# Kernel optimization log

Hardware: AMD Instinct MI355X
Metric: run time of the kernel (lower is better)

## Reference

```python
import jax, jax.numpy as jnp
from jax import lax
import numpy as np

DN = ('NCHW', 'OIHW', 'NCHW')


def conv(x, w, b, pad=0):
    y = lax.conv_general_dilated(x, w, (1, 1), [(pad, pad), (pad, pad)],
                                 dimension_numbers=DN)
    return y + b[None, :, None, None]


def deconv(x, w, b, stride=1):
    # PyTorch ConvTranspose2d weight is (in, out, kH, kW); equivalent conv uses
    # flipped, in/out-transposed kernel with lhs dilation = stride, pad = k-1.
    k = w.shape[2]
    wt = jnp.flip(w, (2, 3)).transpose(1, 0, 2, 3)
    y = lax.conv_general_dilated(x, wt, (1, 1), [(k - 1, k - 1), (k - 1, k - 1)],
                                 lhs_dilation=(stride, stride), dimension_numbers=DN)
    return y + b[None, :, None, None]


def maxpool2(x):
    return lax.reduce_window(x, -jnp.inf, lax.max, (1, 1, 2, 2), (1, 1, 2, 2), 'VALID')


def setup_inputs() -> dict:
    key = jax.random.key(0)
    ks = jax.random.split(key, 12)
    B = 256

    def he(k, shape, fan_in):
        return jax.random.normal(k, shape, jnp.float32) * np.sqrt(2.0 / fan_in)

    inp = {
        'x': jax.random.normal(ks[0], (B, 1, 28, 28), jnp.float32),
        # encoder convs
        'w1': he(ks[1], (128, 1, 5, 5), 1 * 25), 'b1': jnp.zeros((128,), jnp.float32),
        'w2': he(ks[2], (128, 128, 5, 5), 128 * 25), 'b2': jnp.zeros((128,), jnp.float32),
        'w3': he(ks[3], (128, 128, 5, 5), 128 * 25), 'b3': jnp.zeros((128,), jnp.float32),
        # decoder transposed convs (torch shape: in, out, kH, kW)
        't1w': he(ks[4], (128, 128, 4, 4), 128 * 16), 't1b': jnp.zeros((128,), jnp.float32),
        't2w': he(ks[5], (128, 128, 4, 4), 128 * 16), 't2b': jnp.zeros((128,), jnp.float32),
        't3w': he(ks[6], (128, 128, 5, 5), 128 * 25), 't3b': jnp.zeros((128,), jnp.float32),
        't4w': he(ks[7], (128, 128, 5, 5), 128 * 25), 't4b': jnp.zeros((128,), jnp.float32),
        # mu_net 1x1 conv
        'mw': he(ks[8], (1, 128, 1, 1), 128), 'mb': jnp.zeros((1,), jnp.float32),
        # codebook: Embedding(128, 128), init ~ N(0, 1)
        'dict_w': jax.random.normal(ks[9], (128, 128), jnp.float32),
    }
    return inp


def reference(x, w1, b1, w2, b2, w3, b3,
              t1w, t1b, t2w, t2b, t3w, t3b, t4w, t4b,
              mw, mb, dict_w):
    BETA, RATE = 0.25, 5.0
    # ---- encoder ----
    h = jax.nn.relu(conv(x, w1, b1, pad=0))          # (B,128,24,24)
    h = jax.nn.relu(conv(h, w2, b2, pad=2))          # (B,128,24,24)
    h = maxpool2(h)                                  # (B,128,12,12)
    h = conv(h, w3, b3, pad=2)                       # (B,128,12,12)
    z = maxpool2(h)                                  # (B,128,6,6)

    # ---- nearest_neighbor (faithful: argmax of distance, as in the source) ----
    z_sg = lax.stop_gradient(z)
    z2 = jnp.sum(z_sg * z_sg, axis=1, keepdims=True)          # (B,1,6,6)
    w2n = jnp.sum(dict_w * dict_w, axis=1)                     # (K,)
    cross = jnp.einsum('bchw,kc->bkhw', z_sg, lax.stop_gradient(dict_w))
    d2 = z2 + w2n[None, :, None, None] - 2.0 * cross           # (B,K,6,6)
    index = jnp.argmax(d2, axis=1)                             # (B,6,6) int

    # ---- embedding gather ----
    val = dict_w[index].transpose(0, 3, 1, 2)                  # (B,128,6,6)

    # ---- decoder on detached codes ----
    f = lax.stop_gradient(val)
    f = jax.nn.relu(deconv(f, t1w, t1b, stride=1))             # (B,128,9,9)
    f = jax.nn.relu(deconv(f, t2w, t2b, stride=2))             # (B,128,20,20)
    f = jax.nn.relu(deconv(f, t3w, t3b, stride=1))             # (B,128,24,24)
    f = jax.nn.relu(deconv(f, t4w, t4b, stride=1))             # (B,128,28,28)
    mu = conv(f, mw, mb, pad=0)                                # (B,1,28,28)

    loss_rec = jnp.mean((mu - x) ** 2)
    dict_loss = jnp.mean((val - lax.stop_gradient(z)) ** 2) * RATE
    enc_loss = jnp.mean((z - lax.stop_gradient(val)) ** 2) * BETA * RATE
    var_loss = jnp.zeros((), jnp.float32)
    losses = jnp.stack([loss_rec, dict_loss, enc_loss, var_loss])
    return losses, index
```

## Files before the change

kernel.cpp:

```cpp
#include <hip/hip_runtime.h>
#include <hip/hip_bf16.h>


#define B_ 256

typedef __attribute__((ext_vector_type(8))) short s16x8;
typedef __attribute__((ext_vector_type(4))) short s16x4;
typedef __attribute__((ext_vector_type(8))) _Float16 f16x8;
typedef __attribute__((ext_vector_type(4))) float f32x4;

__device__ inline ushort f2bf(float f) {
  union { __hip_bfloat16 h; ushort u; } cv;
  cv.h = __float2bfloat16(f);
  return cv.u;
}

__global__ __launch_bounds__(256) void prep_all(
    const float* __restrict__ t1w, const float* __restrict__ t3w,
    const float* __restrict__ t4w, const float* __restrict__ t2w,
    const float* __restrict__ w2, const float* __restrict__ w3,
    ushort* __restrict__ wp1, ushort* __restrict__ wp3,
    ushort* __restrict__ wp4, ushort* __restrict__ wp2,
    _Float16* __restrict__ w2h, _Float16* __restrict__ w2l,
    _Float16* __restrict__ w3h, _Float16* __restrict__ w3l) {
  const int b = blockIdx.x, t = threadIdx.x;
  if (b < 1024) {
    int idx = b * 256 + t;
    int ci = idx & 127, co = (idx >> 7) & 127, tap = idx >> 14;
    wp1[idx] = f2bf(t1w[((size_t)ci * 128 + co) * 16 + (15 - tap)]);
  } else if (b < 2624) {
    int idx = (b - 1024) * 256 + t;
    int ci = idx & 127, co = (idx >> 7) & 127, tap = idx >> 14;
    wp3[idx] = f2bf(t3w[((size_t)ci * 128 + co) * 25 + (24 - tap)]);
  } else if (b < 4224) {
    int idx = (b - 2624) * 256 + t;
    int ci = idx & 127, co = (idx >> 7) & 127, tap = idx >> 14;
    wp4[idx] = f2bf(t4w[((size_t)ci * 128 + co) * 25 + (24 - tap)]);
  } else if (b < 5248) {
    int idx = (b - 4224) * 256 + t;
    int ci = idx & 127, co = (idx >> 7) & 127;
    int tap = (idx >> 14) & 3, pp = idx >> 16;
    int u = tap >> 1, v = tap & 1, py = pp >> 1, px = pp & 1;
    wp2[idx] = f2bf(
        t2w[(((size_t)ci * 128 + co) * 4 + (py + 2 * u)) * 4 + (px + 2 * v)]);
  } else if (b < 6848) {
    int idx = (b - 5248) * 256 + t;
    int ci = idx & 127, co = (idx >> 7) & 127, tap = idx >> 14;
    float v = w2[((size_t)co * 128 + ci) * 25 + tap];
    _Float16 h = (_Float16)v;
    w2h[idx] = h;
    w2l[idx] = (_Float16)(v - (float)h);
  } else {
    int idx = (b - 6848) * 256 + t;
    int ci = idx & 127, co = (idx >> 7) & 127, tap = idx >> 14;
    float v = w3[((size_t)co * 128 + ci) * 25 + tap];
    _Float16 h = (_Float16)v;
    w3h[idx] = h;
    w3l[idx] = (_Float16)(v - (float)h);
  }
}

__global__ __launch_bounds__(256) void conv1_kernel(
    const float* __restrict__ x, const float* __restrict__ w,
    const float* __restrict__ b, _Float16* __restrict__ oh,
    _Float16* __restrict__ ol) {
  const int n = blockIdx.x;
  __shared__ float xl[784];
  __shared__ float wl[128 * 25];
  __shared__ float bl[128];
  const int t = threadIdx.x;
  for (int e = t; e < 784; e += 256) xl[e] = x[n * 784 + e];
  for (int e = t; e < 3200; e += 256) wl[e] = w[e];
  if (t < 128) bl[t] = b[t];
  __syncthreads();
  const size_t nb = (size_t)n * 73728;
  for (int idx = t; idx < 73728; idx += 256) {
    int co = idx & 127, p = idx >> 7;
    int y = p / 24, xx = p % 24;
    float acc = bl[co];
    const float* wc = &wl[co * 25];
#pragma unroll
    for (int ky = 0; ky < 5; ky++)
#pragma unroll
      for (int kx = 0; kx < 5; kx++)
        acc += xl[(y + ky) * 28 + xx + kx] * wc[ky * 5 + kx];
    float v = fmaxf(acc, 0.f);
    _Float16 h = (_Float16)v;
    oh[nb + idx] = h;
    ol[nb + idx] = (_Float16)(v - (float)h);
  }
}

template <int IW, int K, int PAD, int TR, bool RELU, bool OUT_F32, int PWX>
__global__ __launch_bounds__(256, 3) void conv_mfma_pool(
    const _Float16* __restrict__ inh, const _Float16* __restrict__ inl,
    const _Float16* __restrict__ wph, const _Float16* __restrict__ wpl,
    const float* __restrict__ bias, _Float16* __restrict__ outh,
    _Float16* __restrict__ outl, float* __restrict__ outf) {
  constexpr int IH = IW, OW = IW, OH = IW;
  constexpr int PW = PWX;
  constexpr int SROWS = TR + K - 1;
  constexpr int S = SROWS * PW;
  constexpr int NPOS = TR * OW;
  constexpr int NCH = NPOS / 16;
  constexpr int SCRP = NPOS + 1;
  constexpr int K2 = K * K;
  constexpr int PITCH = 40;
  constexpr int LIN_ELT = S * PITCH;
  constexpr int LIN_BYTES = 2 * LIN_ELT * 2;
  constexpr int SCR_BYTES = 64 * SCRP * 4;
  constexpr int SMEM_BYTES = LIN_BYTES > SCR_BYTES ? LIN_BYTES : SCR_BYTES;
  static_assert(NPOS % 16 == 0, "");
  static_assert(TR % 2 == 0 && OW % 2 == 0, "");
  static_assert(PW >= OW + K - 1, "");
  __shared__ __align__(16) char smem[SMEM_BYTES];
  _Float16* linh = (_Float16*)smem;
  _Float16* linl = linh + LIN_ELT;
  const int n = blockIdx.x;
  const int r0 = blockIdx.y * TR;
  const int t = threadIdx.x;
  const int wv = t >> 6;
  const int lane = t & 63;
  const int nn = lane & 15;
  const int q = lane >> 4;
  f32x4 acc0[NCH], acc1[NCH];
  int boff[NCH];
#pragma unroll
  for (int c = 0; c < NCH; c++) {
    acc0[c] = f32x4{0.f, 0.f, 0.f, 0.f};
    acc1[c] = f32x4{0.f, 0.f, 0.f, 0.f};
    int p = c * 16 + nn;
    boff[c] = ((p / OW) * PW + (p % OW)) * PITCH + q * 8;
  }
  const int rowA = wv * 16 + nn;
  const int rowB = (wv + 4) * 16 + nn;
  for (int cb = 0; cb < 4; cb++) {
    const int ci0 = cb * 32;
    __syncthreads();
    for (int e = t; e < S * 4; e += 256) {
      int sp = e >> 2, j = e & 3;
      int r = sp / PW, c = sp - r * PW;
      int ir = r0 + r - PAD, ic = c - PAD;
      f16x8 vh = {0, 0, 0, 0, 0, 0, 0, 0};
      f16x8 vl = {0, 0, 0, 0, 0, 0, 0, 0};
      if (ir >= 0 && ir < IH && ic >= 0 && ic < IW) {
        size_t g = ((size_t)n * (IH * IW) + ir * IW + ic) * 128 + ci0 + j * 8;
        vh = *(const f16x8*)&inh[g];
        vl = *(const f16x8*)&inl[g];
      }
      int st = sp * PITCH + j * 8;
      *(f16x8*)&linh[st] = vh;
      *(f16x8*)&linl[st] = vl;
    }
    __syncthreads();
    const size_t gA = (size_t)rowA * 128 + ci0 + q * 8;
    const size_t gB = (size_t)rowB * 128 + ci0 + q * 8;
    f16x8 cah0 = *(const f16x8*)&wph[gA];
    f16x8 cal0 = *(const f16x8*)&wpl[gA];
    f16x8 cah1 = *(const f16x8*)&wph[gB];
    f16x8 cal1 = *(const f16x8*)&wpl[gB];
    for (int tap = 0; tap < K2; tap++) {
      f16x8 nah0 = cah0, nal0 = cal0, nah1 = cah1, nal1 = cal1;
      if (tap + 1 < K2) {
        size_t oA = gA + (size_t)(tap + 1) * 16384;
        size_t oB = gB + (size_t)(tap + 1) * 16384;
        nah0 = *(const f16x8*)&wph[oA];
        nal0 = *(const f16x8*)&wpl[oA];
        nah1 = *(const f16x8*)&wph[oB];
        nal1 = *(const f16x8*)&wpl[oB];
      }
      const int ky = tap / K, kx = tap - ky * K;
      const int tp = (ky * PW + kx) * PITCH;
#pragma unroll
      for (int c = 0; c < NCH; c++) {
        int off = boff[c] + tp;
        f16x8 bh = *(const f16x8*)&linh[off];
        f16x8 bl = *(const f16x8*)&linl[off];
        acc0[c] =
            __builtin_amdgcn_mfma_f32_16x16x32_f16(cah0, bh, acc0[c], 0, 0, 0);
        acc0[c] =
            __builtin_amdgcn_mfma_f32_16x16x32_f16(cah0, bl, acc0[c], 0, 0, 0);
        acc0[c] =
            __builtin_amdgcn_mfma_f32_16x16x32_f16(cal0, bh, acc0[c], 0, 0, 0);
        acc1[c] =
            __builtin_amdgcn_mfma_f32_16x16x32_f16(cah1, bh, acc1[c], 0, 0, 0);
        acc1[c] =
            __builtin_amdgcn_mfma_f32_16x16x32_f16(cah1, bl, acc1[c], 0, 0, 0);
        acc1[c] =
            __builtin_amdgcn_mfma_f32_16x16x32_f16(cal1, bh, acc1[c], 0, 0, 0);
      }
      cah0 = nah0; cal0 = nal0; cah1 = nah1; cal1 = nal1;
    }
  }
  __syncthreads();
  float* scr = (float*)smem + wv * 16 * SCRP;
#pragma unroll
  for (int j = 0; j < 2; j++) {
    const int cot = (j ? wv + 4 : wv) * 16;
#pragma unroll
    for (int c = 0; c < NCH; c++) {
      f32x4 a = j ? acc1[c] : acc0[c];
#pragma unroll
      for (int r = 0; r < 4; r++) {
        float v = a[r] + bias[cot + q * 4 + r];
        if (RELU) v = fmaxf(v, 0.f);
        scr[(q * 4 + r) * SCRP + c * 16 + nn] = v;
      }
    }
    __syncthreads();
    for (int e = lane; e < 16 * (TR / 2) * (OW / 2); e += 64) {
      int co_l = e & 15;
      int rem = e >> 4;
      int pr = rem / (OW / 2), pc = rem - pr * (OW / 2);
      const float* s = scr + co_l * SCRP;
      int lp = (2 * pr) * OW + 2 * pc;
      float m =
          fmaxf(fmaxf(s[lp], s[lp + 1]), fmaxf(s[lp + OW], s[lp + OW + 1]));
      int sp_out = (r0 / 2 + pr) * (OW / 2) + pc;
      size_t go =
          ((size_t)n * ((OH / 2) * (OW / 2)) + sp_out) * 128 + cot + co_l;
      if (OUT_F32) {
        outf[go] = m;
      } else {
        _Float16 h = (_Float16)m;
        outh[go] = h;
        outl[go] = (_Float16)(m - (float)h);
      }
    }
    __syncthreads();
  }
}

__global__ __launch_bounds__(256) void vq_kernel(
    const float* __restrict__ z, const float* __restrict__ dict,
    float* __restrict__ val, ushort* __restrict__ val_bf,
    float* __restrict__ out_idx) {
  const int n = blockIdx.x;
  __shared__ float zl[36 * 128];
  __shared__ float d2[36 * 129];
  __shared__ float w2n[128];
  __shared__ int bk[36];
  const int t = threadIdx.x;
  const float* zn = z + (size_t)n * 4608;
  for (int e = t; e < 4608; e += 256) zl[e] = zn[e];
  if (t < 128) {
    float s = 0.f;
    const float* wr = dict + t * 128;
    for (int c = 0; c < 128; c++) s += wr[c] * wr[c];
    w2n[t] = s;
  }
  __syncthreads();
  const int k = t & 127, pg = t >> 7;
  float dot[18];
#pragma unroll
  for (int i = 0; i < 18; i++) dot[i] = 0.f;
  const float* wr = dict + k * 128;
  for (int c = 0; c < 128; c++) {
    float wv = wr[c];
#pragma unroll
    for (int i = 0; i < 18; i++) dot[i] += zl[(pg * 18 + i) * 128 + c] * wv;
  }
  float wn = w2n[k];
#pragma unroll
  for (int i = 0; i < 18; i++) d2[(pg * 18 + i) * 129 + k] = wn - 2.f * dot[i];
  __syncthreads();
  if (t < 36) {
    const float* dr = &d2[t * 129];
    float best = dr[0];
    int bi = 0;
    for (int kk = 1; kk < 128; kk++) {
      float v = dr[kk];
      if (v > best) { best = v; bi = kk; }
    }
    bk[t] = bi;
    out_idx[n * 36 + t] = (float)bi;
  }
  __syncthreads();
  float* vn = val + (size_t)n * 4608;
  ushort* vbn = val_bf + (size_t)n * 4608;
  for (int e = t; e < 4608; e += 256) {
    int c = e & 127, p = e >> 7;
    float v = dict[bk[p] * 128 + c];
    vn[e] = v;
    vbn[e] = f2bf(v);
  }
}

template <int IH, int IW, int OH, int OW, int K, int TR, bool MU_FUSE, int PWX>
__global__ __attribute__((amdgpu_flat_work_group_size(256, 256),
                          amdgpu_waves_per_eu(2, 2))) void deconv_mfma(
    const ushort* __restrict__ in, const ushort* __restrict__ wprep,
    const float* __restrict__ bias, const float* __restrict__ mw,
    void* __restrict__ outp) {
  constexpr int PAD = K - 1;
  constexpr int PW = PWX;
  constexpr int K2 = K * K;
  constexpr int SROWS = TR + K - 1;
  constexpr int S = SROWS * PW;
  constexpr int NPOS = TR * OW;
  constexpr int NCH = (NPOS + 15) / 16;
  constexpr int NT0 = (NCH + 1) / 2;
  constexpr int NT1 = NCH - NT0;
  constexpr int PITCH = 40;
  constexpr int LIN_ELT = S * PITCH;
  constexpr int NSTG = (S * 4 + 255) / 256;
  static_assert(PW >= OW + K - 1, "");
  __shared__ __align__(16) ushort lin[2][LIN_ELT];
  const int n = blockIdx.x;
  const int r0 = blockIdx.y * TR;
  const int t = threadIdx.x;
  const int wv = t >> 6;
  const int lane = t & 63;
  const int nn = lane & 15;
  const int q = lane >> 4;
  const int pairid = wv >> 1;
  const int cohalf = wv & 1;
  f32x4 acc[NT0][4];
  int boff[NT0];
#pragma unroll
  for (int tL = 0; tL < NT0; tL++) {
#pragma unroll
    for (int g = 0; g < 4; g++) acc[tL][g] = f32x4{0.f, 0.f, 0.f, 0.f};
    int tg = pairid * NT0 + tL;
    if (tg > NCH - 1) tg = NCH - 1;
    int p = tg * 16 + nn;
    int pc = p < NPOS ? p : NPOS - 1;
    boff[tL] = ((pc / OW) * PW + (pc % OW)) * PITCH + q * 8;
  }
  s16x8 stg[NSTG];
  auto load_stage = [&](int ci0) {
#pragma unroll
    for (int i = 0; i < NSTG; i++) {
      int e = t + i * 256;
      s16x8 v = {0, 0, 0, 0, 0, 0, 0, 0};
      if (e < S * 4) {
        int sp = e >> 2, j = e & 3;
        int rr = sp / PW, cc = sp - rr * PW;
        int ir = r0 + rr - PAD, ic = cc - PAD;
        if (ir >= 0 && ir < IH && ic >= 0 && ic < IW)
          v = *(const s16x8*)&in[((size_t)n * (IH * IW) + ir * IW + ic) * 128 +
                                 ci0 + j * 8];
      }
      stg[i] = v;
    }
  };
  auto store_stage = [&](int bsel) {
#pragma unroll
    for (int i = 0; i < NSTG; i++) {
      int e = t + i * 256;
      if (e < S * 4) {
        int sp = e >> 2, j = e & 3;
        *(s16x8*)&lin[bsel][sp * PITCH + j * 8] = stg[i];
      }
    }
  };

  load_stage(0);
  store_stage(0);
  __syncthreads();
  for (int cb = 0; cb < 4; cb++) {
    const int ci0 = cb * 32;
    if (cb < 3) load_stage(ci0 + 32);
    const ushort* L = lin[cb & 1];
    size_t gA[4];
#pragma unroll
    for (int g = 0; g < 4; g++)
      gA[g] = (size_t)(cohalf * 64 + g * 16 + nn) * 128 + ci0 + q * 8;
    s16x8 ca[4];
#pragma unroll
    for (int g = 0; g < 4; g++) ca[g] = *(const s16x8*)&wprep[gA[g]];
    for (int tap = 0; tap < K2; tap++) {
      s16x8 na[4];
#pragma unroll
      for (int g = 0; g < 4; g++) na[g] = ca[g];
      if (tap + 1 < K2) {
        const size_t to = (size_t)(tap + 1) * 16384;
#pragma unroll
        for (int g = 0; g < 4; g++)
          na[g] = *(const s16x8*)&wprep[gA[g] + to];
      }
      const int ky = tap / K, kx = tap - ky * K;
      const int tp = (ky * PW + kx) * PITCH;
#pragma unroll
      for (int tL = 0; tL < NT0; tL++) {
        if (pairid == 0 || tL < NT1) {
          s16x8 b = *(const s16x8*)&L[boff[tL] + tp];
#pragma unroll
          for (int g = 0; g < 4; g++)
            acc[tL][g] = __builtin_amdgcn_mfma_f32_16x16x32_bf16(ca[g], b,
                                                                acc[tL][g], 0,
                                                                0, 0);
        }
      }
#pragma unroll
      for (int g = 0; g < 4; g++) ca[g] = na[g];
    }
    if (cb < 3) {
      store_stage((cb + 1) & 1);
      __syncthreads();
    }
  }
  float bav[4][4];
#pragma unroll
  for (int g = 0; g < 4; g++)
#pragma unroll
    for (int r = 0; r < 4; r++)
      bav[g][r] = bias[cohalf * 64 + g * 16 + q * 4 + r];
  if (!MU_FUSE) {
    ushort* out = (ushort*)outp;
#pragma unroll
    for (int tL = 0; tL < NT0; tL++) {
      if (pairid == 0 || tL < NT1) {
        int tg = pairid * NT0 + tL;
        int p = tg * 16 + nn;
        if (p < NPOS) {
          size_t go =
              ((size_t)n * (OH * OW) + r0 * OW + p) * 128 + cohalf * 64;
#pragma unroll
          for (int g = 0; g < 4; g++) {
            s16x4 pk;
#pragma unroll
            for (int r = 0; r < 4; r++)
              pk[r] = (short)f2bf(fmaxf(acc[tL][g][r] + bav[g][r], 0.f));
            *(s16x4*)&out[go + g * 16 + q * 4] = pk;
          }
        }
      }
    }
  } else {
    float* out = (float*)outp;
    float mwv[4][4];
#pragma unroll
    for (int g = 0; g < 4; g++)
#pragma unroll
      for (int r = 0; r < 4; r++)
        mwv[g][r] = mw[cohalf * 64 + g * 16 + q * 4 + r];
#pragma unroll
    for (int tL = 0; tL < NT0; tL++) {
      if (pairid == 0 || tL < NT1) {
        int tg = pairid * NT0 + tL;
        int p = tg * 16 + nn;
        float s = 0.f;
#pragma unroll
        for (int g = 0; g < 4; g++)
#pragma unroll
          for (int r = 0; r < 4; r++)
            s += fmaxf(acc[tL][g][r] + bav[g][r], 0.f) * mwv[g][r];
        s += __shfl_xor(s, 16);
        s += __shfl_xor(s, 32);
        if (q == 0 && p < NPOS)
          atomicAdd(&out[(size_t)n * (OH * OW) + r0 * OW + p], s);
      }
    }
  }
}

__global__ __launch_bounds__(256, 3) void deconv_s2_mfma(
    const ushort* __restrict__ in, const ushort* __restrict__ wp2,
    const float* __restrict__ bias, ushort* __restrict__ out) {
  constexpr int NCH = 7;
  constexpr int PITCH = 40;
  constexpr int PW = 18;
  constexpr int S = 11 * PW;
  const int n = blockIdx.x;
  const int pp = blockIdx.y;
  const int py = pp >> 1, px = pp & 1;
  __shared__ __align__(16) ushort lin[S * PITCH];
  const int t = threadIdx.x;
  const int wv = t >> 6;
  const int lane = t & 63;
  const int nn = lane & 15;
  const int q = lane >> 4;
  f32x4 acc0[NCH], acc1[NCH];
  int boff[NCH];
#pragma unroll
  for (int c = 0; c < NCH; c++) {
    acc0[c] = f32x4{0.f, 0.f, 0.f, 0.f};
    acc1[c] = f32x4{0.f, 0.f, 0.f, 0.f};
    int p = c * 16 + nn;
    int pc = p < 100 ? p : 99;
    boff[c] = ((pc / 10) * PW + (pc % 10)) * PITCH + q * 8;
  }
  const int toffs[4] = {PW + 1, PW, 1, 0};
  for (int cb = 0; cb < 4; cb++) {
    const int ci0 = cb * 32;
    __syncthreads();
    for (int e = t; e < S * 4; e += 256) {
      int sp = e >> 2, j = e & 3;
      int r = sp / PW, c2 = sp - r * PW;
      int ir = r - 1, ic = c2 - 1;
      s16x8 v = {0, 0, 0, 0, 0, 0, 0, 0};
      if (ir >= 0 && ir < 9 && ic >= 0 && ic < 9)
        v = *(const s16x8*)&in[((size_t)n * 81 + ir * 9 + ic) * 128 + ci0 +
                               j * 8];
      *(s16x8*)&lin[sp * PITCH + j * 8] = v;
    }
    __syncthreads();
    const size_t gA =
        ((size_t)(pp * 4) * 128 + wv * 16 + nn) * 128 + ci0 + q * 8;
    const size_t gB =
        ((size_t)(pp * 4) * 128 + (wv + 4) * 16 + nn) * 128 + ci0 + q * 8;
    s16x8 ca0 = *(const s16x8*)&wp2[gA];
    s16x8 ca1 = *(const s16x8*)&wp2[gB];
    for (int tap = 0; tap < 4; tap++) {
      s16x8 na0 = ca0, na1 = ca1;
      if (tap + 1 < 4) {
        na0 = *(const s16x8*)&wp2[gA + (size_t)(tap + 1) * 16384];
        na1 = *(const s16x8*)&wp2[gB + (size_t)(tap + 1) * 16384];
      }
      const int tp = toffs[tap] * PITCH;
#pragma unroll
      for (int c = 0; c < NCH; c++) {
        s16x8 b = *(const s16x8*)&lin[boff[c] + tp];
        acc0[c] =
            __builtin_amdgcn_mfma_f32_16x16x32_bf16(ca0, b, acc0[c], 0, 0, 0);
        acc1[c] =
            __builtin_amdgcn_mfma_f32_16x16x32_bf16(ca1, b, acc1[c], 0, 0, 0);
      }
      ca0 = na0; ca1 = na1;
    }
  }
  const int co_a = wv * 16 + q * 4;
  const int co_b = (wv + 4) * 16 + q * 4;
#pragma unroll
  for (int c = 0; c < NCH; c++) {
    int p = c * 16 + nn;
    if (p < 100) {
      int oy = 2 * (p / 10) + py, ox = 2 * (p % 10) + px;
      size_t go = ((size_t)n * 400 + oy * 20 + ox) * 128;
      s16x4 pa, pb;
#pragma unroll
      for (int r = 0; r < 4; r++) {
        pa[r] = (short)f2bf(fmaxf(acc0[c][r] + bias[co_a + r], 0.f));
        pb[r] = (short)f2bf(fmaxf(acc1[c][r] + bias[co_b + r], 0.f));
      }
      *(s16x4*)&out[go + co_a] = pa;
      *(s16x4*)&out[go + co_b] = pb;
    }
  }
}

__global__ __launch_bounds__(256) void loss_kernel(
    const float* __restrict__ mu, const float* __restrict__ mb,
    const float* __restrict__ x, const float4* __restrict__ val4,
    const float4* __restrict__ z4, float* __restrict__ out) {
  const int b = blockIdx.x, t = threadIdx.x;
  __shared__ float red[256];
  if (b < 784) {
    int i = b * 256 + t;
    float d = mu[i] + mb[0] - x[i];
    red[t] = d * d;
  } else {
    int i = (b - 784) * 256 + t;
    float4 a = val4[i], zz = z4[i];
    float dx = a.x - zz.x, dy = a.y - zz.y, dz = a.z - zz.z, dw = a.w - zz.w;
    red[t] = dx * dx + dy * dy + dz * dz + dw * dw;
  }
  __syncthreads();
  for (int off = 128; off > 0; off >>= 1) {
    if (t < off) red[t] += red[t + off];
    __syncthreads();
  }
  if (t == 0) {
    if (b < 784) {
      atomicAdd(out, red[0] * (1.0f / 200704.f));
    } else {
      atomicAdd(out + 1, red[0] * (5.f / 1179648.f));
      atomicAdd(out + 2, red[0] * (1.25f / 1179648.f));
    }
  }
}

extern "C" void kernel_launch(void* const* d_in, const int* in_sizes, int n_in,
                              void* d_out, int out_size, void* d_ws,
                              size_t ws_size, hipStream_t stream) {
  const float* x = (const float*)d_in[0];
  const float* w1 = (const float*)d_in[1];
  const float* b1 = (const float*)d_in[2];
  const float* w2 = (const float*)d_in[3];
  const float* b2 = (const float*)d_in[4];
  const float* w3 = (const float*)d_in[5];
  const float* b3 = (const float*)d_in[6];
  const float* t1w = (const float*)d_in[7];
  const float* t1b = (const float*)d_in[8];
  const float* t2w = (const float*)d_in[9];
  const float* t2b = (const float*)d_in[10];
  const float* t3w = (const float*)d_in[11];
  const float* t3b = (const float*)d_in[12];
  const float* t4w = (const float*)d_in[13];
  const float* t4b = (const float*)d_in[14];
  const float* mw = (const float*)d_in[15];
  const float* mb = (const float*)d_in[16];
  const float* dictw = (const float*)d_in[17];
  float* out = (float*)d_out;

  float* p = (float*)d_ws;
  _Float16* h1h = (_Float16*)p; p += 9437184;
  _Float16* h1l = (_Float16*)p; p += 9437184;
  _Float16* p1h = (_Float16*)p; p += 2359296;
  _Float16* p1l = (_Float16*)p; p += 2359296;
  float* z = p; p += 1179648;
  float* val = p; p += 1179648;
  ushort* val_bf = (ushort*)p; p += 589824;
  float* mu = p; p += 200704;
  ushort* wp1 = (ushort*)p; p += 131072;
  ushort* wp3 = (ushort*)p; p += 204800;
  ushort* wp4 = (ushort*)p; p += 204800;
  ushort* wp2 = (ushort*)p; p += 131072;
  _Float16* w2h = (_Float16*)p; p += 204800;
  _Float16* w2l = (_Float16*)p; p += 204800;
  _Float16* w3h = (_Float16*)p; p += 204800;
  _Float16* w3l = (_Float16*)p; p += 204800;
  ushort* f1 = (ushort*)p1h;
  ushort* f2 = (ushort*)h1l;
  ushort* f3 = (ushort*)h1h;

  hipMemsetAsync(d_out, 0, 4 * sizeof(float), stream);
  hipMemsetAsync(mu, 0, 200704 * sizeof(float), stream);

  prep_all<<<8448, 256, 0, stream>>>(t1w, t3w, t4w, t2w, w2, w3, wp1, wp3, wp4,
                                     wp2, w2h, w2l, w3h, w3l);

  conv1_kernel<<<B_, 256, 0, stream>>>(x, w1, b1, h1h, h1l);
  conv_mfma_pool<24, 5, 2, 6, true, false, 28>
      <<<dim3(B_, 4), 256, 0, stream>>>(h1h, h1l, w2h, w2l, b2, p1h, p1l,
                                        nullptr);
  conv_mfma_pool<12, 5, 2, 4, false, true, 20>
      <<<dim3(B_, 3), 256, 0, stream>>>(p1h, p1l, w3h, w3l, b3, nullptr,
                                        nullptr, z);
  vq_kernel<<<B_, 256, 0, stream>>>(z, dictw, val, val_bf, out + 4);
  deconv_mfma<6, 6, 9, 9, 4, 9, false, 17>
      <<<dim3(B_, 1), 256, 0, stream>>>(val_bf, wp1, t1b, nullptr, f1);
  deconv_s2_mfma<<<dim3(B_, 4), 256, 0, stream>>>(f1, wp2, t2b, f2);
  deconv_mfma<20, 20, 24, 24, 5, 8, false, 28>
      <<<dim3(B_, 3), 256, 0, stream>>>(f2, wp3, t3b, nullptr, f3);
  deconv_mfma<24, 24, 28, 28, 5, 7, true, 36>
      <<<dim3(B_, 4), 256, 0, stream>>>(f3, wp4, t4b, mw, mu);
  loss_kernel<<<1936, 256, 0, stream>>>(mu, mb, x, (const float4*)val,
                                        (const float4*)z, out);
}
```

Measured before the change: 1.031 ms.

## Fuse VQ losses into vq kernel and shrink deconv row tiles for more blocks

```diff
diff --git a/kernel.cpp b/kernel.cpp
--- a/kernel.cpp
+++ b/kernel.cpp
@@ -234,12 +234,13 @@
 __global__ __launch_bounds__(256) void vq_kernel(
     const float* __restrict__ z, const float* __restrict__ dict,
     float* __restrict__ val, ushort* __restrict__ val_bf,
-    float* __restrict__ out_idx) {
+    float* __restrict__ out_idx, float* __restrict__ out) {
   const int n = blockIdx.x;
   __shared__ float zl[36 * 128];
   __shared__ float d2[36 * 129];
   __shared__ float w2n[128];
   __shared__ int bk[36];
+  __shared__ float red[256];
   const int t = threadIdx.x;
   const float* zn = z + (size_t)n * 4608;
   for (int e = t; e < 4608; e += 256) zl[e] = zn[e];
@@ -278,17 +279,29 @@
   __syncthreads();
   float* vn = val + (size_t)n * 4608;
   ushort* vbn = val_bf + (size_t)n * 4608;
+  float lsum = 0.f;
   for (int e = t; e < 4608; e += 256) {
     int c = e & 127, p = e >> 7;
     float v = dict[bk[p] * 128 + c];
     vn[e] = v;
     vbn[e] = f2bf(v);
+    float d = v - zl[e];
+    lsum += d * d;
+  }
+  red[t] = lsum;
+  __syncthreads();
+  for (int off = 128; off > 0; off >>= 1) {
+    if (t < off) red[t] += red[t + off];
+    __syncthreads();
+  }
+  if (t == 0) {
+    atomicAdd(out + 1, red[0] * (5.f / 1179648.f));
+    atomicAdd(out + 2, red[0] * (1.25f / 1179648.f));
   }
 }
 
 template <int IH, int IW, int OH, int OW, int K, int TR, bool MU_FUSE, int PWX>
-__global__ __attribute__((amdgpu_flat_work_group_size(256, 256),
-                          amdgpu_waves_per_eu(2, 2))) void deconv_mfma(
+__global__ __launch_bounds__(256, 2) void deconv_mfma(
     const ushort* __restrict__ in, const ushort* __restrict__ wprep,
     const float* __restrict__ bias, const float* __restrict__ mw,
     void* __restrict__ outp) {
@@ -542,33 +555,18 @@
 
 __global__ __launch_bounds__(256) void loss_kernel(
     const float* __restrict__ mu, const float* __restrict__ mb,
-    const float* __restrict__ x, const float4* __restrict__ val4,
-    const float4* __restrict__ z4, float* __restrict__ out) {
+    const float* __restrict__ x, float* __restrict__ out) {
   const int b = blockIdx.x, t = threadIdx.x;
   __shared__ float red[256];
-  if (b < 784) {
-    int i = b * 256 + t;
-    float d = mu[i] + mb[0] - x[i];
-    red[t] = d * d;
-  } else {
-    int i = (b - 784) * 256 + t;
-    float4 a = val4[i], zz = z4[i];
-    float dx = a.x - zz.x, dy = a.y - zz.y, dz = a.z - zz.z, dw = a.w - zz.w;
-    red[t] = dx * dx + dy * dy + dz * dz + dw * dw;
-  }
+  int i = b * 256 + t;
+  float d = mu[i] + mb[0] - x[i];
+  red[t] = d * d;
   __syncthreads();
   for (int off = 128; off > 0; off >>= 1) {
     if (t < off) red[t] += red[t + off];
     __syncthreads();
   }
-  if (t == 0) {
-    if (b < 784) {
-      atomicAdd(out, red[0] * (1.0f / 200704.f));
-    } else {
-      atomicAdd(out + 1, red[0] * (5.f / 1179648.f));
-      atomicAdd(out + 2, red[0] * (1.25f / 1179648.f));
-    }
-  }
+  if (t == 0) atomicAdd(out, red[0] * (1.0f / 200704.f));
 }
 
 extern "C" void kernel_launch(void* const* d_in, const int* in_sizes, int n_in,
@@ -628,14 +626,13 @@
   conv_mfma_pool<12, 5, 2, 4, false, true, 20>
       <<<dim3(B_, 3), 256, 0, stream>>>(p1h, p1l, w3h, w3l, b3, nullptr,
                                         nullptr, z);
-  vq_kernel<<<B_, 256, 0, stream>>>(z, dictw, val, val_bf, out + 4);
-  deconv_mfma<6, 6, 9, 9, 4, 9, false, 17>
-      <<<dim3(B_, 1), 256, 0, stream>>>(val_bf, wp1, t1b, nullptr, f1);
+  vq_kernel<<<B_, 256, 0, stream>>>(z, dictw, val, val_bf, out + 4, out);
+  deconv_mfma<6, 6, 9, 9, 4, 3, false, 17>
+      <<<dim3(B_, 3), 256, 0, stream>>>(val_bf, wp1, t1b, nullptr, f1);
   deconv_s2_mfma<<<dim3(B_, 4), 256, 0, stream>>>(f1, wp2, t2b, f2);
-  deconv_mfma<20, 20, 24, 24, 5, 8, false, 28>
-      <<<dim3(B_, 3), 256, 0, stream>>>(f2, wp3, t3b, nullptr, f3);
-  deconv_mfma<24, 24, 28, 28, 5, 7, true, 36>
-      <<<dim3(B_, 4), 256, 0, stream>>>(f3, wp4, t4b, mw, mu);
-  loss_kernel<<<1936, 256, 0, stream>>>(mu, mb, x, (const float4*)val,
-                                        (const float4*)z, out);
-}
+  deconv_mfma<20, 20, 24, 24, 5, 4, false, 28>
+      <<<dim3(B_, 6), 256, 0, stream>>>(f2, wp3, t3b, nullptr, f3);
+  deconv_mfma<24, 24, 28, 28, 5, 4, true, 36>
+      <<<dim3(B_, 7), 256, 0, stream>>>(f3, wp4, t4b, mw, mu);
+  loss_kernel<<<784, 256, 0, stream>>>(mu, mb, x, out);
+}
```

Measured after the change: 1.292 ms. +25.3%, slower.
